# Performance work log

Measured on AMD Instinct MI355X. Metric: run time of the kernel, lower is better.

## Reference

```python
import jax, jax.numpy as jnp
import numpy as np

N = 50000      # number of predictions
E = 1_600_000  # total neighborhood entries (sum of neighborhood sizes)
D = 128        # prediction representation dim
A = 4          # additional per-pair info dim (box offsets / IoU)
H = 128        # block hidden dim


def setup_inputs() -> dict:
    key = jax.random.key(0)
    ks = jax.random.split(key, 16)
    interpolated = jax.random.normal(ks[0], (N, D), dtype=jnp.float32)
    add_info = jax.random.normal(ks[1], (E, A), dtype=jnp.float32)
    neighbor_idx = jax.random.randint(ks[2], (E,), 0, N, dtype=jnp.int32)
    segment_ids = jnp.sort(jax.random.randint(ks[3], (E,), 0, N, dtype=jnp.int32))
    w = lambda k, shape: (jax.random.normal(k, shape, dtype=jnp.float32) * 0.02)
    return {
        "interpolated": interpolated,
        "add_info": add_info,
        "neighbor_idx": neighbor_idx,
        "segment_ids": segment_ids,
        "Wb0": w(ks[4], (D + A, H)), "bb0": jnp.zeros((H,), jnp.float32),
        "Wo0": w(ks[5], (H, D)),     "bo0": jnp.zeros((D,), jnp.float32),
        "Wb1": w(ks[6], (D + A, H)), "bb1": jnp.zeros((H,), jnp.float32),
        "Wo1": w(ks[7], (H, D)),     "bo1": jnp.zeros((D,), jnp.float32),
        "Wf": w(ks[8], (D, 1)),      "bf": jnp.zeros((1,), jnp.float32),
    }


def reference(interpolated, add_info, neighbor_idx, segment_ids,
              Wb0, bb0, Wo0, bo0, Wb1, bb1, Wo1, bo1, Wf, bf):
    def block_step(feats, Wb, bb, Wo, bo):
        # assemble all neighborhoods: gather neighbor reps, concat pair info -> (E, D+A)
        edge_feats = jnp.concatenate([feats[neighbor_idx], add_info], axis=-1)
        # block MLP on neighborhood entries -> (E, H)
        h = jax.nn.relu(edge_feats @ Wb + bb)
        # segment-wise max pool over each prediction's neighborhood -> (N, H)
        pooled = jax.ops.segment_max(h, segment_ids, num_segments=N)
        pooled = jnp.where(jnp.isfinite(pooled), pooled, 0.0)  # empty segments -> 0
        # output projection back to representation space, residual update
        return feats + (pooled @ Wo + bo)

    x = block_step(interpolated, Wb0, bb0, Wo0, bo0)
    x = block_step(x, Wb1, bb1, Wo1, bo1)
    # final layers: compress representation to updated objectness score -> (N, 1)
    return x @ Wf + bf
```

## Files before the change

### kernel.cpp

```cpp
#include <hip/hip_runtime.h>
#include <limits.h>
#include <cstdint>

typedef __bf16 bf16_t;
typedef __attribute__((ext_vector_type(8))) __bf16 bf16x8;
typedef __attribute__((ext_vector_type(4))) float f32x4;
typedef __attribute__((ext_vector_type(2))) float f32x2;

#define CH 64

struct PackArgs {
  const float* W[4];
  bf16_t* P[4];
};

__global__ __launch_bounds__(256) void pack4_kernel(PackArgs args) {
  int idx = blockIdx.x * blockDim.x + threadIdx.x;
  int which = idx >> 14;
  int r = idx & 16383;
  int j  = r & 7;
  int L  = (r >> 3) & 63;
  int nt = (r >> 9) & 7;
  int kt = r >> 12;
  int k = kt * 32 + (L >> 4) * 8 + j;
  int n = nt * 16 + (L & 15);
  args.P[which][r] = (bf16_t)args.W[which][(size_t)k * 128 + n];
}

__global__ __launch_bounds__(256, 4) void yproj_f32(
    const float* __restrict__ X, const bf16_t* __restrict__ Wtpk,
    bf16_t* __restrict__ Ybf, float* __restrict__ pooled, int N)
{
  const int tid = threadIdx.x;
  const int base = blockIdx.x * 128;

  float4 z = make_float4(0.f, 0.f, 0.f, 0.f);
  #pragma unroll
  for (int i = 0; i < 16; ++i) {
    int idx = tid + i * 256;
    int row = base + (idx >> 5);
    if (row < N)
      reinterpret_cast<float4*>(pooled)[(size_t)row * 32 + (idx & 31)] = z;
  }

  const int lane = tid & 63;
  const int w    = tid >> 6;
  const int q    = lane >> 4;
  const int ln   = lane & 15;
  const int n0   = base + w * 32;

  int r0 = n0 + ln, r1 = n0 + 16 + ln;
  int r0c = (r0 < N) ? r0 : (N - 1);
  int r1c = (r1 < N) ? r1 : (N - 1);
  const float* x0 = X + (size_t)r0c * 128 + q * 8;
  const float* x1 = X + (size_t)r1c * 128 + q * 8;

  f32x4 acc[2][8];
  #pragma unroll
  for (int mt = 0; mt < 2; ++mt)
    #pragma unroll
    for (int nt = 0; nt < 8; ++nt)
      #pragma unroll
      for (int r = 0; r < 4; ++r) acc[mt][nt][r] = 0.f;

  const bf16x8* Wp = reinterpret_cast<const bf16x8*>(Wtpk);
  #pragma unroll
  for (int kt = 0; kt < 4; ++kt) {
    float4 f0a = *reinterpret_cast<const float4*>(x0 + kt * 32);
    float4 f0b = *reinterpret_cast<const float4*>(x0 + kt * 32 + 4);
    float4 f1a = *reinterpret_cast<const float4*>(x1 + kt * 32);
    float4 f1b = *reinterpret_cast<const float4*>(x1 + kt * 32 + 4);
    bf16x8 a0, a1;
    a0[0] = (bf16_t)f0a.x; a0[1] = (bf16_t)f0a.y; a0[2] = (bf16_t)f0a.z; a0[3] = (bf16_t)f0a.w;
    a0[4] = (bf16_t)f0b.x; a0[5] = (bf16_t)f0b.y; a0[6] = (bf16_t)f0b.z; a0[7] = (bf16_t)f0b.w;
    a1[0] = (bf16_t)f1a.x; a1[1] = (bf16_t)f1a.y; a1[2] = (bf16_t)f1a.z; a1[3] = (bf16_t)f1a.w;
    a1[4] = (bf16_t)f1b.x; a1[5] = (bf16_t)f1b.y; a1[6] = (bf16_t)f1b.z; a1[7] = (bf16_t)f1b.w;
    #pragma unroll
    for (int nt = 0; nt < 8; ++nt) {
      bf16x8 bfrag = Wp[(kt * 8 + nt) * 64 + lane];
      acc[0][nt] = __builtin_amdgcn_mfma_f32_16x16x32_bf16(a0, bfrag, acc[0][nt], 0, 0, 0);
      acc[1][nt] = __builtin_amdgcn_mfma_f32_16x16x32_bf16(a1, bfrag, acc[1][nt], 0, 0, 0);
    }
  }

  #pragma unroll
  for (int mt = 0; mt < 2; ++mt) {
    #pragma unroll
    for (int r = 0; r < 4; ++r) {
      int row = n0 + mt * 16 + q * 4 + r;
      if (row < N) {
        #pragma unroll
        for (int nt = 0; nt < 8; ++nt) {
          int col = nt * 16 + ln;
          Ybf[(size_t)row * 128 + col] = (bf16_t)acc[mt][nt][r];
        }
      }
    }
  }
}

__global__ __launch_bounds__(256) void edge_stream(
    const bf16_t* __restrict__ Y,
    const float* __restrict__ Wb,
    const float* __restrict__ bb,
    const float* __restrict__ add_info,
    const int* __restrict__ nbr, const int* __restrict__ segs,
    float* __restrict__ pooled, int E)
{
  __shared__ float a_lds[1024];
  const int lane = threadIdx.x & 63;
  const int wv = __builtin_amdgcn_readfirstlane(threadIdx.x >> 6);
  const int e0 = (blockIdx.x * 4 + wv) * CH;
  if (e0 >= E) return;
  const int c0 = lane * 2;

  f32x2 wk[4];
  #pragma unroll
  for (int k = 0; k < 4; ++k) {
    wk[k].x = Wb[(size_t)(128 + k) * 128 + c0];
    wk[k].y = Wb[(size_t)(128 + k) * 128 + c0 + 1];
  }
  f32x2 bbv;
  bbv.x = bb[c0]; bbv.y = bb[c0 + 1];

  unsigned* pooled_u = reinterpret_cast<unsigned*>(pooled);
  f32x2 v; v.x = 0.f; v.y = 0.f;

  if (e0 + CH <= E) {
    float4 av = *reinterpret_cast<const float4*>(add_info + (size_t)e0 * 4 + lane * 4);
    int v_nbr = nbr[e0 + lane];
    int v_sg  = segs[e0 + lane];

    int sg_prev = __shfl_up(v_sg, 1);
    unsigned long long bmask = __ballot(v_sg != sg_prev) & ~1ull;
    int cur = __builtin_amdgcn_readlane(v_sg, 0);

    unsigned ybuf[4][8];
    #pragma unroll
    for (int p = 0; p < 3; ++p) {
      #pragma unroll
      for (int j = 0; j < 8; ++j) {
        int rn = __builtin_amdgcn_readlane(v_nbr, p * 8 + j);
        ybuf[p][j] = *((const unsigned*)(Y + (size_t)rn * 128) + lane);
      }
    }

    *reinterpret_cast<float4*>(a_lds + wv * 256 + lane * 4) = av;

    #pragma unroll
    for (int g = 0; g < CH / 8; ++g) {
      if (g + 3 < CH / 8) {
        #pragma unroll
        for (int j = 0; j < 8; ++j) {
          int rn = __builtin_amdgcn_readlane(v_nbr, (g + 3) * 8 + j);
          ybuf[(g + 3) & 3][j] = *((const unsigned*)(Y + (size_t)rn * 128) + lane);
        }
      }
      #pragma unroll
      for (int j = 0; j < 8; ++j) {
        const int i = g * 8 + j;
        if (bmask & (1ull << i)) {
          if (v.x > 0.f) atomicMax(&pooled_u[(size_t)cur * 128 + c0], __float_as_uint(v.x));
          if (v.y > 0.f) atomicMax(&pooled_u[(size_t)cur * 128 + c0 + 1], __float_as_uint(v.y));
          v.x = 0.f; v.y = 0.f;
          cur = __builtin_amdgcn_readlane(v_sg, i);
        }
        unsigned yb = ybuf[g & 3][j];
        f32x2 y;
        y.x = __uint_as_float(yb << 16);
        y.y = __uint_as_float(yb & 0xffff0000u);
        f32x4 a4 = *reinterpret_cast<const f32x4*>(a_lds + wv * 256 + i * 4);
        f32x2 t = bbv + a4[0] * wk[0];
        t += a4[1] * wk[1];
        t += a4[2] * wk[2];
        t += a4[3] * wk[3];
        t += y;
        v = __builtin_elementwise_max(v, t);
      }
    }
    if (v.x > 0.f) atomicMax(&pooled_u[(size_t)cur * 128 + c0], __float_as_uint(v.x));
    if (v.y > 0.f) atomicMax(&pooled_u[(size_t)cur * 128 + c0 + 1], __float_as_uint(v.y));
  } else {
    int cur = segs[e0];
    const int rem = E - e0;
    for (int i = 0; i < rem; ++i) {
      const int e = e0 + i;
      int sg = segs[e];
      if (sg != cur) {
        if (v.x > 0.f) atomicMax(&pooled_u[(size_t)cur * 128 + c0], __float_as_uint(v.x));
        if (v.y > 0.f) atomicMax(&pooled_u[(size_t)cur * 128 + c0 + 1], __float_as_uint(v.y));
        v.x = 0.f; v.y = 0.f; cur = sg;
      }
      unsigned yb = *reinterpret_cast<const unsigned*>(Y + (size_t)nbr[e] * 128 + c0);
      float y0 = __uint_as_float(yb << 16);
      float y1 = __uint_as_float(yb & 0xffff0000u);
      const float* ai = add_info + (size_t)e * 4;
      float a0 = ai[0], a1 = ai[1], a2 = ai[2], a3 = ai[3];
      float t0 = y0 + bbv.x + a0 * wk[0].x + a1 * wk[1].x + a2 * wk[2].x + a3 * wk[3].x;
      float t1 = y1 + bbv.y + a0 * wk[0].y + a1 * wk[1].y + a2 * wk[2].y + a3 * wk[3].y;
      v.x = fmaxf(v.x, t0);
      v.y = fmaxf(v.y, t1);
    }
    if (v.x > 0.f) atomicMax(&pooled_u[(size_t)cur * 128 + c0], __float_as_uint(v.x));
    if (v.y > 0.f) atomicMax(&pooled_u[(size_t)cur * 128 + c0 + 1], __float_as_uint(v.y));
  }
}

__global__ __launch_bounds__(256, 4) void update_yproj(
    const float* featsIn, float* pooled,
    const bf16_t* __restrict__ Wopk, const float* __restrict__ bo,
    const bf16_t* __restrict__ Wtpk,
    float* __restrict__ featsOut, bf16_t* __restrict__ Ybf, int N)
{
  __shared__ bf16_t fb[128][136];

  const int tid  = threadIdx.x;
  const int lane = tid & 63;
  const int w    = tid >> 6;
  const int q    = lane >> 4;
  const int ln   = lane & 15;
  const int base = blockIdx.x * 128;
  const int n0   = base + w * 32;

  int r0 = n0 + ln, r1 = n0 + 16 + ln;
  int r0c = (r0 < N) ? r0 : (N - 1);
  int r1c = (r1 < N) ? r1 : (N - 1);
  const float* p0 = pooled + (size_t)r0c * 128 + q * 8;
  const float* p1 = pooled + (size_t)r1c * 128 + q * 8;

  f32x4 acc[2][8];
  #pragma unroll
  for (int mt = 0; mt < 2; ++mt)
    #pragma unroll
    for (int nt = 0; nt < 8; ++nt)
      #pragma unroll
      for (int r = 0; r < 4; ++r) acc[mt][nt][r] = 0.f;

  const bf16x8* Wp = reinterpret_cast<const bf16x8*>(Wopk);
  #pragma unroll
  for (int kt = 0; kt < 4; ++kt) {
    float4 f0a = *reinterpret_cast<const float4*>(p0 + kt * 32);
    float4 f0b = *reinterpret_cast<const float4*>(p0 + kt * 32 + 4);
    float4 f1a = *reinterpret_cast<const float4*>(p1 + kt * 32);
    float4 f1b = *reinterpret_cast<const float4*>(p1 + kt * 32 + 4);
    bf16x8 a0, a1;
    a0[0] = (bf16_t)f0a.x; a0[1] = (bf16_t)f0a.y; a0[2] = (bf16_t)f0a.z; a0[3] = (bf16_t)f0a.w;
    a0[4] = (bf16_t)f0b.x; a0[5] = (bf16_t)f0b.y; a0[6] = (bf16_t)f0b.z; a0[7] = (bf16_t)f0b.w;
    a1[0] = (bf16_t)f1a.x; a1[1] = (bf16_t)f1a.y; a1[2] = (bf16_t)f1a.z; a1[3] = (bf16_t)f1a.w;
    a1[4] = (bf16_t)f1b.x; a1[5] = (bf16_t)f1b.y; a1[6] = (bf16_t)f1b.z; a1[7] = (bf16_t)f1b.w;
    #pragma unroll
    for (int nt = 0; nt < 8; ++nt) {
      bf16x8 bfrag = Wp[(kt * 8 + nt) * 64 + lane];
      acc[0][nt] = __builtin_amdgcn_mfma_f32_16x16x32_bf16(a0, bfrag, acc[0][nt], 0, 0, 0);
      acc[1][nt] = __builtin_amdgcn_mfma_f32_16x16x32_bf16(a1, bfrag, acc[1][nt], 0, 0, 0);
    }
  }

  float bov[8];
  #pragma unroll
  for (int nt = 0; nt < 8; ++nt) bov[nt] = bo[nt * 16 + ln];

  #pragma unroll
  for (int mt = 0; mt < 2; ++mt) {
    #pragma unroll
    for (int r = 0; r < 4; ++r) {
      int row  = n0 + mt * 16 + q * 4 + r;
      int lrow = w * 32 + mt * 16 + q * 4 + r;
      if (row < N) {
        #pragma unroll
        for (int nt = 0; nt < 8; ++nt) {
          int col = nt * 16 + ln;
          float o = featsIn[(size_t)row * 128 + col] + acc[mt][nt][r] + bov[nt];
          featsOut[(size_t)row * 128 + col] = o;
          fb[lrow][col] = (bf16_t)o;
        }
      } else {
        #pragma unroll
        for (int nt = 0; nt < 8; ++nt) fb[lrow][nt * 16 + ln] = (bf16_t)0.f;
      }
    }
  }

  __syncthreads();

  float4 z = make_float4(0.f, 0.f, 0.f, 0.f);
  #pragma unroll
  for (int i = 0; i < 16; ++i) {
    int idx = tid + i * 256;
    int row = base + (idx >> 5);
    if (row < N)
      reinterpret_cast<float4*>(pooled)[(size_t)row * 32 + (idx & 31)] = z;
  }

  f32x4 acc2[2][8];
  #pragma unroll
  for (int mt = 0; mt < 2; ++mt)
    #pragma unroll
    for (int nt = 0; nt < 8; ++nt)
      #pragma unroll
      for (int r = 0; r < 4; ++r) acc2[mt][nt][r] = 0.f;

  const bf16x8* Wp2 = reinterpret_cast<const bf16x8*>(Wtpk);
  const int lrow0 = w * 32 + ln;
  const int lrow1 = lrow0 + 16;
  #pragma unroll
  for (int kt = 0; kt < 4; ++kt) {
    bf16x8 a0 = *reinterpret_cast<const bf16x8*>(&fb[lrow0][q * 8 + kt * 32]);
    bf16x8 a1 = *reinterpret_cast<const bf16x8*>(&fb[lrow1][q * 8 + kt * 32]);
    #pragma unroll
    for (int nt = 0; nt < 8; ++nt) {
      bf16x8 bfrag = Wp2[(kt * 8 + nt) * 64 + lane];
      acc2[0][nt] = __builtin_amdgcn_mfma_f32_16x16x32_bf16(a0, bfrag, acc2[0][nt], 0, 0, 0);
      acc2[1][nt] = __builtin_amdgcn_mfma_f32_16x16x32_bf16(a1, bfrag, acc2[1][nt], 0, 0, 0);
    }
  }

  #pragma unroll
  for (int mt = 0; mt < 2; ++mt) {
    #pragma unroll
    for (int r = 0; r < 4; ++r) {
      int row = n0 + mt * 16 + q * 4 + r;
      if (row < N) {
        #pragma unroll
        for (int nt = 0; nt < 8; ++nt) {
          int col = nt * 16 + ln;
          Ybf[(size_t)row * 128 + col] = (bf16_t)acc2[mt][nt][r];
        }
      }
    }
  }
}

__global__ __launch_bounds__(256, 4) void update_final_mfma(
    const float* __restrict__ featsIn, const float* __restrict__ pooled,
    const bf16_t* __restrict__ Wopk, const float* __restrict__ bo,
    const float* __restrict__ Wf, const float* __restrict__ bf_,
    float* __restrict__ out, int N)
{
  const int tid  = threadIdx.x;
  const int lane = tid & 63;
  const int w    = tid >> 6;
  const int q    = lane >> 4;
  const int ln   = lane & 15;
  const int n0   = blockIdx.x * 128 + w * 32;

  int r0 = n0 + ln, r1 = n0 + 16 + ln;
  int r0c = (r0 < N) ? r0 : (N - 1);
  int r1c = (r1 < N) ? r1 : (N - 1);
  const float* p0 = pooled + (size_t)r0c * 128 + q * 8;
  const float* p1 = pooled + (size_t)r1c * 128 + q * 8;

  f32x4 acc[2][8];
  #pragma unroll
  for (int mt = 0; mt < 2; ++mt)
    #pragma unroll
    for (int nt = 0; nt < 8; ++nt)
      #pragma unroll
      for (int r = 0; r < 4; ++r) acc[mt][nt][r] = 0.f;

  const bf16x8* Wp = reinterpret_cast<const bf16x8*>(Wopk);
  #pragma unroll
  for (int kt = 0; kt < 4; ++kt) {
    float4 f0a = *reinterpret_cast<const float4*>(p0 + kt * 32);
    float4 f0b = *reinterpret_cast<const float4*>(p0 + kt * 32 + 4);
    float4 f1a = *reinterpret_cast<const float4*>(p1 + kt * 32);
    float4 f1b = *reinterpret_cast<const float4*>(p1 + kt * 32 + 4);
    bf16x8 a0, a1;
    a0[0] = (bf16_t)f0a.x; a0[1] = (bf16_t)f0a.y; a0[2] = (bf16_t)f0a.z; a0[3] = (bf16_t)f0a.w;
    a0[4] = (bf16_t)f0b.x; a0[5] = (bf16_t)f0b.y; a0[6] = (bf16_t)f0b.z; a0[7] = (bf16_t)f0b.w;
    a1[0] = (bf16_t)f1a.x; a1[1] = (bf16_t)f1a.y; a1[2] = (bf16_t)f1a.z; a1[3] = (bf16_t)f1a.w;
    a1[4] = (bf16_t)f1b.x; a1[5] = (bf16_t)f1b.y; a1[6] = (bf16_t)f1b.z; a1[7] = (bf16_t)f1b.w;
    #pragma unroll
    for (int nt = 0; nt < 8; ++nt) {
      bf16x8 bfrag = Wp[(kt * 8 + nt) * 64 + lane];
      acc[0][nt] = __builtin_amdgcn_mfma_f32_16x16x32_bf16(a0, bfrag, acc[0][nt], 0, 0, 0);
      acc[1][nt] = __builtin_amdgcn_mfma_f32_16x16x32_bf16(a1, bfrag, acc[1][nt], 0, 0, 0);
    }
  }

  float bov[8], wfv[8];
  #pragma unroll
  for (int nt = 0; nt < 8; ++nt) { bov[nt] = bo[nt * 16 + ln]; wfv[nt] = Wf[nt * 16 + ln]; }
  float bfs = bf_[0];

  #pragma unroll
  for (int mt = 0; mt < 2; ++mt) {
    #pragma unroll
    for (int r = 0; r < 4; ++r) {
      int row = n0 + mt * 16 + q * 4 + r;
      float partial = 0.f;
      if (row < N) {
        #pragma unroll
        for (int nt = 0; nt < 8; ++nt) {
          int col = nt * 16 + ln;
          float o = featsIn[(size_t)row * 128 + col] + acc[mt][nt][r] + bov[nt];
          partial += o * wfv[nt];
        }
      }
      partial += __shfl_xor(partial, 1);
      partial += __shfl_xor(partial, 2);
      partial += __shfl_xor(partial, 4);
      partial += __shfl_xor(partial, 8);
      if (ln == 0 && row < N) out[row] = partial + bfs;
    }
  }
}

extern "C" void kernel_launch(void* const* d_in, const int* in_sizes, int n_in,
                              void* d_out, int out_size, void* d_ws, size_t ws_size,
                              hipStream_t stream)
{
  const float* interpolated = (const float*)d_in[0];
  const float* add_info     = (const float*)d_in[1];
  const int*   nbr          = (const int*)d_in[2];
  const int*   segs         = (const int*)d_in[3];
  const float* Wb0 = (const float*)d_in[4];
  const float* bb0 = (const float*)d_in[5];
  const float* Wo0 = (const float*)d_in[6];
  const float* bo0 = (const float*)d_in[7];
  const float* Wb1 = (const float*)d_in[8];
  const float* bb1 = (const float*)d_in[9];
  const float* Wo1 = (const float*)d_in[10];
  const float* bo1 = (const float*)d_in[11];
  const float* Wf  = (const float*)d_in[12];
  const float* bf_ = (const float*)d_in[13];

  const int N = in_sizes[0] / 128;
  const int E = in_sizes[2];
  float* out = (float*)d_out;

  float* pooled = (float*)d_ws;
  float* featsB = pooled + (size_t)N * 128;
  bf16_t* Ybf   = (bf16_t*)(featsB + (size_t)N * 128);
  bf16_t* Wtpk0 = Ybf + (size_t)N * 128;
  bf16_t* Wtpk1 = Wtpk0 + 16384;
  bf16_t* Wopk0 = Wtpk1 + 16384;
  bf16_t* Wopk1 = Wopk0 + 16384;

  const int ugrid = (N + 127) / 128;
  const int egrid = (E + CH * 4 - 1) / (CH * 4);

  PackArgs pa;
  pa.W[0] = Wb0; pa.P[0] = Wtpk0;
  pa.W[1] = Wb1; pa.P[1] = Wtpk1;
  pa.W[2] = Wo0; pa.P[2] = Wopk0;
  pa.W[3] = Wo1; pa.P[3] = Wopk1;
  pack4_kernel<<<256, 256, 0, stream>>>(pa);

  yproj_f32<<<ugrid, 256, 0, stream>>>(interpolated, Wtpk0, Ybf, pooled, N);
  edge_stream<<<egrid, 256, 0, stream>>>(Ybf, Wb0, bb0, add_info, nbr, segs,
                                         pooled, E);
  update_yproj<<<ugrid, 256, 0, stream>>>(interpolated, pooled, Wopk0, bo0,
                                          Wtpk1, featsB, Ybf, N);

  edge_stream<<<egrid, 256, 0, stream>>>(Ybf, Wb1, bb1, add_info, nbr, segs,
                                         pooled, E);
  update_final_mfma<<<ugrid, 256, 0, stream>>>(featsB, pooled, Wopk1, bo1,
                                               Wf, bf_, out, N);
}
```

Measured before the change: 310.0 us.

## Replace stored intermediate features with per-row Wf dot and use single-wave blocks

The first update kernel no longer writes the full fp32 intermediate feature matrix. It computes only its dot product with Wf per row (fdot), and the final kernel adds that scalar to the projection of the second residual term, which follows from linearity of the final layer. This removes one N×128 fp32 write and one read. The node kernels also move from 256-thread blocks of 128 rows to 64-thread single-wave blocks of 32 rows, and the pooled zeroing moves after the MFMA phase behind an explicit wait, which drops the block-wide barrier. The trade-off is four times as many blocks and more redundant per-block weight fragment loads.

```diff
diff --git a/kernel.cpp b/kernel.cpp
--- a/kernel.cpp
+++ b/kernel.cpp
@@ -27,29 +27,26 @@
   args.P[which][r] = (bf16_t)args.W[which][(size_t)k * 128 + n];
 }
 
-__global__ __launch_bounds__(256, 4) void yproj_f32(
+__global__ __launch_bounds__(64) void yproj_f32(
     const float* __restrict__ X, const bf16_t* __restrict__ Wtpk,
     bf16_t* __restrict__ Ybf, float* __restrict__ pooled, int N)
 {
-  const int tid = threadIdx.x;
-  const int base = blockIdx.x * 128;
+  const int lane = threadIdx.x;
+  const int base = blockIdx.x * 32;
 
   float4 z = make_float4(0.f, 0.f, 0.f, 0.f);
   #pragma unroll
   for (int i = 0; i < 16; ++i) {
-    int idx = tid + i * 256;
+    int idx = lane + i * 64;
     int row = base + (idx >> 5);
     if (row < N)
       reinterpret_cast<float4*>(pooled)[(size_t)row * 32 + (idx & 31)] = z;
   }
 
-  const int lane = tid & 63;
-  const int w    = tid >> 6;
-  const int q    = lane >> 4;
-  const int ln   = lane & 15;
-  const int n0   = base + w * 32;
-
-  int r0 = n0 + ln, r1 = n0 + 16 + ln;
+  const int q  = lane >> 4;
+  const int ln = lane & 15;
+
+  int r0 = base + ln, r1 = base + 16 + ln;
   int r0c = (r0 < N) ? r0 : (N - 1);
   int r1c = (r1 < N) ? r1 : (N - 1);
   const float* x0 = X + (size_t)r0c * 128 + q * 8;
@@ -87,7 +84,7 @@
   for (int mt = 0; mt < 2; ++mt) {
     #pragma unroll
     for (int r = 0; r < 4; ++r) {
-      int row = n0 + mt * 16 + q * 4 + r;
+      int row = base + mt * 16 + q * 4 + r;
       if (row < N) {
         #pragma unroll
         for (int nt = 0; nt < 8; ++nt) {
@@ -206,23 +203,20 @@
   }
 }
 
-__global__ __launch_bounds__(256, 4) void update_yproj(
+__global__ __launch_bounds__(64) void update_yproj(
     const float* featsIn, float* pooled,
     const bf16_t* __restrict__ Wopk, const float* __restrict__ bo,
-    const bf16_t* __restrict__ Wtpk,
-    float* __restrict__ featsOut, bf16_t* __restrict__ Ybf, int N)
+    const bf16_t* __restrict__ Wtpk, const float* __restrict__ Wf,
+    float* __restrict__ fdot, bf16_t* __restrict__ Ybf, int N)
 {
-  __shared__ bf16_t fb[128][136];
-
-  const int tid  = threadIdx.x;
-  const int lane = tid & 63;
-  const int w    = tid >> 6;
+  __shared__ bf16_t fb[32][136];
+
+  const int lane = threadIdx.x;
   const int q    = lane >> 4;
   const int ln   = lane & 15;
-  const int base = blockIdx.x * 128;
-  const int n0   = base + w * 32;
-
-  int r0 = n0 + ln, r1 = n0 + 16 + ln;
+  const int base = blockIdx.x * 32;
+
+  int r0 = base + ln, r1 = base + 16 + ln;
   int r0c = (r0 < N) ? r0 : (N - 1);
   int r1c = (r1 < N) ? r1 : (N - 1);
   const float* p0 = pooled + (size_t)r0c * 128 + q * 8;
@@ -256,40 +250,35 @@
     }
   }
 
-  float bov[8];
-  #pragma unroll
-  for (int nt = 0; nt < 8; ++nt) bov[nt] = bo[nt * 16 + ln];
+  float bov[8], wfv[8];
+  #pragma unroll
+  for (int nt = 0; nt < 8; ++nt) { bov[nt] = bo[nt * 16 + ln]; wfv[nt] = Wf[nt * 16 + ln]; }
 
   #pragma unroll
   for (int mt = 0; mt < 2; ++mt) {
     #pragma unroll
     for (int r = 0; r < 4; ++r) {
-      int row  = n0 + mt * 16 + q * 4 + r;
-      int lrow = w * 32 + mt * 16 + q * 4 + r;
+      int row  = base + mt * 16 + q * 4 + r;
+      int lrow = mt * 16 + q * 4 + r;
+      float partial = 0.f;
       if (row < N) {
         #pragma unroll
         for (int nt = 0; nt < 8; ++nt) {
           int col = nt * 16 + ln;
           float o = featsIn[(size_t)row * 128 + col] + acc[mt][nt][r] + bov[nt];
-          featsOut[(size_t)row * 128 + col] = o;
           fb[lrow][col] = (bf16_t)o;
+          partial += o * wfv[nt];
         }
       } else {
         #pragma unroll
         for (int nt = 0; nt < 8; ++nt) fb[lrow][nt * 16 + ln] = (bf16_t)0.f;
       }
-    }
-  }
-
-  __syncthreads();
-
-  float4 z = make_float4(0.f, 0.f, 0.f, 0.f);
-  #pragma unroll
-  for (int i = 0; i < 16; ++i) {
-    int idx = tid + i * 256;
-    int row = base + (idx >> 5);
-    if (row < N)
-      reinterpret_cast<float4*>(pooled)[(size_t)row * 32 + (idx & 31)] = z;
+      partial += __shfl_xor(partial, 1);
+      partial += __shfl_xor(partial, 2);
+      partial += __shfl_xor(partial, 4);
+      partial += __shfl_xor(partial, 8);
+      if (ln == 0 && row < N) fdot[row] = partial;
+    }
   }
 
   f32x4 acc2[2][8];
@@ -301,12 +290,10 @@
       for (int r = 0; r < 4; ++r) acc2[mt][nt][r] = 0.f;
 
   const bf16x8* Wp2 = reinterpret_cast<const bf16x8*>(Wtpk);
-  const int lrow0 = w * 32 + ln;
-  const int lrow1 = lrow0 + 16;
   #pragma unroll
   for (int kt = 0; kt < 4; ++kt) {
-    bf16x8 a0 = *reinterpret_cast<const bf16x8*>(&fb[lrow0][q * 8 + kt * 32]);
-    bf16x8 a1 = *reinterpret_cast<const bf16x8*>(&fb[lrow1][q * 8 + kt * 32]);
+    bf16x8 a0 = *reinterpret_cast<const bf16x8*>(&fb[ln][q * 8 + kt * 32]);
+    bf16x8 a1 = *reinterpret_cast<const bf16x8*>(&fb[16 + ln][q * 8 + kt * 32]);
     #pragma unroll
     for (int nt = 0; nt < 8; ++nt) {
       bf16x8 bfrag = Wp2[(kt * 8 + nt) * 64 + lane];
@@ -319,7 +306,7 @@
   for (int mt = 0; mt < 2; ++mt) {
     #pragma unroll
     for (int r = 0; r < 4; ++r) {
-      int row = n0 + mt * 16 + q * 4 + r;
+      int row = base + mt * 16 + q * 4 + r;
       if (row < N) {
         #pragma unroll
         for (int nt = 0; nt < 8; ++nt) {
@@ -329,22 +316,31 @@
       }
     }
   }
-}
-
-__global__ __launch_bounds__(256, 4) void update_final_mfma(
-    const float* __restrict__ featsIn, const float* __restrict__ pooled,
+
+  asm volatile("s_waitcnt vmcnt(0)" ::: "memory");
+  __builtin_amdgcn_sched_barrier(0);
+  float4 z = make_float4(0.f, 0.f, 0.f, 0.f);
+  #pragma unroll
+  for (int i = 0; i < 16; ++i) {
+    int idx = lane + i * 64;
+    int row = base + (idx >> 5);
+    if (row < N)
+      reinterpret_cast<float4*>(pooled)[(size_t)row * 32 + (idx & 31)] = z;
+  }
+}
+
+__global__ __launch_bounds__(64) void update_final_mfma(
+    const float* __restrict__ fdot, const float* __restrict__ pooled,
     const bf16_t* __restrict__ Wopk, const float* __restrict__ bo,
     const float* __restrict__ Wf, const float* __restrict__ bf_,
     float* __restrict__ out, int N)
 {
-  const int tid  = threadIdx.x;
-  const int lane = tid & 63;
-  const int w    = tid >> 6;
+  const int lane = threadIdx.x;
   const int q    = lane >> 4;
   const int ln   = lane & 15;
-  const int n0   = blockIdx.x * 128 + w * 32;
-
-  int r0 = n0 + ln, r1 = n0 + 16 + ln;
+  const int base = blockIdx.x * 32;
+
+  int r0 = base + ln, r1 = base + 16 + ln;
   int r0c = (r0 < N) ? r0 : (N - 1);
   int r1c = (r1 < N) ? r1 : (N - 1);
   const float* p0 = pooled + (size_t)r0c * 128 + q * 8;
@@ -387,21 +383,16 @@
   for (int mt = 0; mt < 2; ++mt) {
     #pragma unroll
     for (int r = 0; r < 4; ++r) {
-      int row = n0 + mt * 16 + q * 4 + r;
+      int row = base + mt * 16 + q * 4 + r;
       float partial = 0.f;
-      if (row < N) {
-        #pragma unroll
-        for (int nt = 0; nt < 8; ++nt) {
-          int col = nt * 16 + ln;
-          float o = featsIn[(size_t)row * 128 + col] + acc[mt][nt][r] + bov[nt];
-          partial += o * wfv[nt];
-        }
-      }
+      #pragma unroll
+      for (int nt = 0; nt < 8; ++nt)
+        partial += (acc[mt][nt][r] + bov[nt]) * wfv[nt];
       partial += __shfl_xor(partial, 1);
       partial += __shfl_xor(partial, 2);
       partial += __shfl_xor(partial, 4);
       partial += __shfl_xor(partial, 8);
-      if (ln == 0 && row < N) out[row] = partial + bfs;
+      if (ln == 0 && row < N) out[row] = partial + fdot[row] + bfs;
     }
   }
 }
@@ -430,14 +421,14 @@
   float* out = (float*)d_out;
 
   float* pooled = (float*)d_ws;
-  float* featsB = pooled + (size_t)N * 128;
-  bf16_t* Ybf   = (bf16_t*)(featsB + (size_t)N * 128);
+  float* fdot   = pooled + (size_t)N * 128;
+  bf16_t* Ybf   = (bf16_t*)(fdot + N);
   bf16_t* Wtpk0 = Ybf + (size_t)N * 128;
   bf16_t* Wtpk1 = Wtpk0 + 16384;
   bf16_t* Wopk0 = Wtpk1 + 16384;
   bf16_t* Wopk1 = Wopk0 + 16384;
 
-  const int ugrid = (N + 127) / 128;
+  const int ugrid = (N + 31) / 32;
   const int egrid = (E + CH * 4 - 1) / (CH * 4);
 
   PackArgs pa;
@@ -447,14 +438,14 @@
   pa.W[3] = Wo1; pa.P[3] = Wopk1;
   pack4_kernel<<<256, 256, 0, stream>>>(pa);
 
-  yproj_f32<<<ugrid, 256, 0, stream>>>(interpolated, Wtpk0, Ybf, pooled, N);
+  yproj_f32<<<ugrid, 64, 0, stream>>>(interpolated, Wtpk0, Ybf, pooled, N);
   edge_stream<<<egrid, 256, 0, stream>>>(Ybf, Wb0, bb0, add_info, nbr, segs,
                                          pooled, E);
-  update_yproj<<<ugrid, 256, 0, stream>>>(interpolated, pooled, Wopk0, bo0,
-                                          Wtpk1, featsB, Ybf, N);
+  update_yproj<<<ugrid, 64, 0, stream>>>(interpolated, pooled, Wopk0, bo0,
+                                         Wtpk1, Wf, fdot, Ybf, N);
 
   edge_stream<<<egrid, 256, 0, stream>>>(Ybf, Wb1, bb1, add_info, nbr, segs,
                                          pooled, E);
-  update_final_mfma<<<ugrid, 256, 0, stream>>>(featsB, pooled, Wopk1, bo1,
-                                               Wf, bf_, out, N);
-}
+  update_final_mfma<<<ugrid, 64, 0, stream>>>(fdot, pooled, Wopk1, bo1,
+                                              Wf, bf_, out, N);
+}
```

Measured after the change: 323.1 us. 4.2% more time.
